# Performance work log

Hardware: AMD Instinct MI355X
Metric: run time of the kernel (lower is better)

The kernel has to match this reference:

```python
import jax, jax.numpy as jnp
import numpy as np

NUM_CODES = 8192
CODE_DIM = 256
BETA = 0.25


def setup_inputs() -> dict:
    key = jax.random.key(0)
    k1, k2 = jax.random.split(key)
    z_e = jax.random.normal(k1, (32, 1024, CODE_DIM), dtype=jnp.float32)
    # matches nn.init.uniform_(weight, -1/num_codes, 1/num_codes)
    codebook = jax.random.uniform(
        k2, (NUM_CODES, CODE_DIM), dtype=jnp.float32,
        minval=-1.0 / NUM_CODES, maxval=1.0 / NUM_CODES)
    return {"z_e": z_e, "codebook": codebook}


def reference(z_e, codebook):
    b, n, d = z_e.shape
    z_flat = z_e.reshape(-1, d)                       # [B*N, D]
    # squared L2 distance via ||z||^2 - 2 z.e + ||e||^2
    z_sq = jnp.sum(z_flat * z_flat, axis=1, keepdims=True)      # [B*N, 1]
    e_sq = jnp.sum(codebook * codebook, axis=1)[None, :]         # [1, K]
    ze = z_flat @ codebook.T                                     # [B*N, K]
    dist = z_sq - 2.0 * ze + e_sq
    codes_idx = jnp.argmin(dist, axis=1)                         # [B*N]
    z_q = codebook[codes_idx].reshape(b, n, d)
    # straight-through estimator
    z_q_st = z_e + jax.lax.stop_gradient(z_q - z_e)
    vq_loss = (jnp.mean((jax.lax.stop_gradient(z_q) - z_e) ** 2)
               + BETA * jnp.mean((z_q - jax.lax.stop_gradient(z_e)) ** 2))
    return z_q_st, vq_loss, codes_idx.reshape(b, n)
```

## Files before the change

### kernel.cpp

```cpp
#include <hip/hip_runtime.h>


#define NUM_CODES 8192
#define DIM 256
#define TOTAL_ROWS 32768
#define ROWS_PER_BLOCK 64
#define TILE_K 32
#define NCHUNK_HALF 128
#define OUT_LOSS_OFF 8388608
#define OUT_IDX_OFF 8388609
#define LOSS_SCALE (1.25 / 8388608.0)
#define DOT_MARGIN 3.5e-4f
#define CLIST_MAX 160

typedef __attribute__((ext_vector_type(8))) short bf16x8;
typedef __attribute__((ext_vector_type(4))) float f32x4;

#define AS1 __attribute__((address_space(1)))
#define AS3 __attribute__((address_space(3)))
static __device__ __forceinline__ void gload_lds16(const void* g, void* l) {
    __builtin_amdgcn_global_load_lds((const AS1 unsigned int*)(uintptr_t)g,
                                     (AS3 unsigned int*)(uintptr_t)l, 16, 0, 0);
}

static __device__ __forceinline__ unsigned short f2bf(float f) {
    union { float f; unsigned u; } v; v.f = f;
    return (unsigned short)((v.u + 0x7FFF + ((v.u >> 16) & 1)) >> 16);
}

static __device__ __forceinline__ float sq32(float v) {
    float s = v * v;
    asm("" : "+v"(s));
    return s;
}

static __device__ __forceinline__ float pairwise256_sq(
        const float* __restrict__ base, int l) {
    const int h = (l >> 3) & 1, j = l & 7;
    const float* p = base + h * 128 + j;
    float acc = sq32(p[0]);
    #pragma unroll
    for (int m = 1; m < 16; ++m) acc += sq32(p[m * 8]);
    acc += __shfl_xor(acc, 1);
    acc += __shfl_xor(acc, 2);
    acc += __shfl_xor(acc, 4);
    acc += __shfl_xor(acc, 8);
    return acc;
}

__global__ __launch_bounds__(64) void rowsq_kernel(const float* __restrict__ x,
                                                   float* __restrict__ sq) {
    const int l = threadIdx.x;
    const long row = ((long)blockIdx.x << 2) + (l >> 4);
    float s = pairwise256_sq(x + row * DIM, l);
    if ((l & 15) == 0) sq[row] = s;
}

__global__ __launch_bounds__(256) void cvt_swz_kernel(
        const float* __restrict__ cb, uint4* __restrict__ pbz) {
    const int o = blockIdx.x * 256 + threadIdx.x;
    const int ch = o >> 10, idx = o & 1023;
    const int c = idx >> 5, sw = idx & 31;
    const int s = sw ^ (c & 7);
    const float* p = cb + ((long)(ch * TILE_K + c) << 8) + s * 8;
    float4 a = *(const float4*)p, b = *(const float4*)(p + 4);
    union { unsigned short us[8]; uint4 v; } r;
    r.us[0] = f2bf(a.x); r.us[1] = f2bf(a.y); r.us[2] = f2bf(a.z); r.us[3] = f2bf(a.w);
    r.us[4] = f2bf(b.x); r.us[5] = f2bf(b.y); r.us[6] = f2bf(b.z); r.us[7] = f2bf(b.w);
    pbz[o] = r.v;
}

__global__ __launch_bounds__(128, 2) void vq_scan_kernel(
        const float* __restrict__ z, const float* __restrict__ cb,
        const uint4* __restrict__ pbz, const float* __restrict__ esq,
        unsigned long long* __restrict__ gwin) {
    __shared__ bf16x8 ct[2][TILE_K * 32];
    __shared__ float zsql[ROWS_PER_BLOCK];
    __shared__ unsigned clist[2][CLIST_MAX];
    __shared__ int ccnt[2];

    const int tid = threadIdx.x;
    const int w = tid >> 6, l = tid & 63;
    const int cl = l & 15, g = l >> 4;
    const int x7 = cl & 7;
    const int rowblk = blockIdx.x & 511;
    const int half = blockIdx.x >> 9;
    const int ch0 = half * NCHUNK_HALF;
    const long rowbase = (long)rowblk * ROWS_PER_BLOCK;
    const int wrowL = w * 32;

    if (l == 0) ccnt[w] = 0;

    #define STAGE(gch_, buf_) { \
        const char* gs_ = (const char*)pbz + ((long)(gch_) << 14) + (w << 10) + (l << 4); \
        char* ld_ = (char*)&ct[buf_][0] + (w << 10); \
        _Pragma("unroll") \
        for (int i_ = 0; i_ < 8; ++i_) \
            gload_lds16(gs_ + i_ * 2048, ld_ + i_ * 2048); \
    }

    STAGE(ch0, 0);

    bf16x8 af[2][8];
    #pragma unroll
    for (int t = 0; t < 2; ++t) {
        const long r = rowbase + wrowL + t * 16 + cl;
        #pragma unroll
        for (int ks = 0; ks < 8; ++ks) {
            const float* p = z + r * DIM + ks * 32 + g * 8;
            float4 a = *(const float4*)p, b = *(const float4*)(p + 4);
            bf16x8 v;
            v[0] = f2bf(a.x); v[1] = f2bf(a.y); v[2] = f2bf(a.z); v[3] = f2bf(a.w);
            v[4] = f2bf(b.x); v[5] = f2bf(b.y); v[6] = f2bf(b.z); v[7] = f2bf(b.w);
            af[t][ks] = v;
        }
    }
    #pragma unroll
    for (int p4 = 0; p4 < 8; ++p4) {
        const int r0 = wrowL + p4 * 4 + (l >> 4);
        float s = pairwise256_sq(z + (rowbase + r0) * DIM, l);
        if ((l & 15) == 0) zsql[r0] = s;
    }
    __syncthreads();

    unsigned k1a[8], k2a[8], k3a[8];
    #pragma unroll
    for (int i = 0; i < 8; ++i) { k1a[i] = 0u; k2a[i] = 0u; k3a[i] = 0u; }

    #define INSERT(rs_, sv_, kc_) { \
        unsigned u_ = __float_as_uint(sv_); \
        u_ ^= ((unsigned)((int)u_ >> 31)) | 0x80000000u; \
        u_ = (u_ & 0xFFFFE000u) | (kc_); \
        unsigned mx_ = k1a[rs_] > u_ ? k1a[rs_] : u_; \
        unsigned mn_ = k1a[rs_] > u_ ? u_ : k1a[rs_]; \
        k1a[rs_] = mx_; \
        unsigned mx2_ = k2a[rs_] > mn_ ? k2a[rs_] : mn_; \
        unsigned mn2_ = k2a[rs_] > mn_ ? mn_ : k2a[rs_]; \
        k2a[rs_] = mx2_; \
        k3a[rs_] = k3a[rs_] > mn2_ ? k3a[rs_] : mn2_; \
    }

    for (int ch = 0; ch < NCHUNK_HALF; ++ch) {
        const int buf = ch & 1;
        if (ch + 1 < NCHUNK_HALF) STAGE(ch0 + ch + 1, buf ^ 1);

        bf16x8 breg[16];
        #pragma unroll
        for (int ks = 0; ks < 8; ++ks)
            #pragma unroll
            for (int nt = 0; nt < 2; ++nt)
                breg[ks * 2 + nt] =
                    ct[buf][nt * 512 + cl * 32 + (((ks << 2) + g) ^ x7)];

        f32x4 acc[2][2];
        #pragma unroll
        for (int t = 0; t < 2; ++t)
            #pragma unroll
            for (int n = 0; n < 2; ++n) acc[t][n] = (f32x4){0.f, 0.f, 0.f, 0.f};
        #pragma unroll
        for (int ks = 0; ks < 8; ++ks) {
            #pragma unroll
            for (int nt = 0; nt < 2; ++nt) {
                acc[0][nt] = __builtin_amdgcn_mfma_f32_16x16x32_bf16(
                    af[0][ks], breg[ks * 2 + nt], acc[0][nt], 0, 0, 0);
                acc[1][nt] = __builtin_amdgcn_mfma_f32_16x16x32_bf16(
                    af[1][ks], breg[ks * 2 + nt], acc[1][nt], 0, 0, 0);
            }
        }

        const unsigned kc0 = (unsigned)((ch0 + ch) * TILE_K + cl);
        #pragma unroll
        for (int t = 0; t < 2; ++t)
            #pragma unroll
            for (int nt = 0; nt < 2; ++nt)
                #pragma unroll
                for (int r = 0; r < 4; ++r)
                    INSERT(t * 4 + r, acc[t][nt][r], nt ? (kc0 + 16) : kc0);

        __syncthreads();
    }

    #define COLLECT(rs_, T_, R_) { \
        unsigned gm_ = k1a[rs_]; \
        unsigned t_; \
        t_ = __shfl_xor(gm_, 1); gm_ = gm_ > t_ ? gm_ : t_; \
        t_ = __shfl_xor(gm_, 2); gm_ = gm_ > t_ ? gm_ : t_; \
        t_ = __shfl_xor(gm_, 4); gm_ = gm_ > t_ ? gm_ : t_; \
        t_ = __shfl_xor(gm_, 8); gm_ = gm_ > t_ ? gm_ : t_; \
        unsigned sb_ = (gm_ & 0x80000000u) ? (gm_ ^ 0x80000000u) : ~gm_; \
        float gs_ = __uint_as_float(sb_) - DOT_MARGIN; \
        unsigned tu_ = __float_as_uint(gs_); \
        tu_ ^= ((unsigned)((int)tu_ >> 31)) | 0x80000000u; \
        tu_ &= 0xFFFFE000u; \
        const unsigned rowp_ = (unsigned)(wrowL + T_ * 16 + g * 4 + R_) << 16; \
        if (k1a[rs_] >= tu_) { int p_ = atomicAdd(&ccnt[w], 1); \
            if (p_ < CLIST_MAX) clist[w][p_] = rowp_ | (k1a[rs_] & 0x1FFFu); } \
        if (k2a[rs_] >= tu_) { int p_ = atomicAdd(&ccnt[w], 1); \
            if (p_ < CLIST_MAX) clist[w][p_] = rowp_ | (k2a[rs_] & 0x1FFFu); } \
        if (k3a[rs_] >= tu_) { int p_ = atomicAdd(&ccnt[w], 1); \
            if (p_ < CLIST_MAX) clist[w][p_] = rowp_ | (k3a[rs_] & 0x1FFFu); } \
    }
    COLLECT(0, 0, 0); COLLECT(1, 0, 1); COLLECT(2, 0, 2); COLLECT(3, 0, 3);
    COLLECT(4, 1, 0); COLLECT(5, 1, 1); COLLECT(6, 1, 2); COLLECT(7, 1, 3);

    const int n = ccnt[w] < CLIST_MAX ? ccnt[w] : CLIST_MAX;
    for (int j = 0; j < n; ++j) {
        const unsigned e = clist[w][j];
        const int rowL = e >> 16;
        const int code = e & 0x1FFF;
        const long grow = rowbase + rowL;
        float4 zz = *(const float4*)(z + grow * DIM + l * 4);
        float4 cc = *(const float4*)(cb + (long)code * DIM + l * 4);
        double dd = (double)zz.x * cc.x + (double)zz.y * cc.y
                  + (double)zz.z * cc.z + (double)zz.w * cc.w;
        dd += __shfl_xor(dd, 1);
        dd += __shfl_xor(dd, 2);
        dd += __shfl_xor(dd, 4);
        dd += __shfl_xor(dd, 8);
        dd += __shfl_xor(dd, 16);
        dd += __shfl_xor(dd, 32);
        const float s = (zsql[rowL] - 2.0f * (float)dd) + esq[code];
        if (l == 0) {
            const unsigned long long p =
                ((unsigned long long)__float_as_uint(s) << 32) | (unsigned)code;
            atomicMin(&gwin[grow], p);
        }
    }
}

__global__ __launch_bounds__(256) void vq_out_kernel(
        const float* __restrict__ z, const float* __restrict__ cb,
        const unsigned long long* __restrict__ gwin,
        float* __restrict__ out, double* __restrict__ loss_acc) {
    const int tid = threadIdx.x;
    const int w = tid >> 6, l = tid & 63;
    const long rowbase = (long)blockIdx.x * ROWS_PER_BLOCK;
    double lacc = 0.0;
    #pragma unroll 1
    for (int i = 0; i < 16; ++i) {
        const long grow = rowbase + w * 16 + i;
        const int kw = (int)(gwin[grow] & 0x1FFFull);
        float4 zz = *(const float4*)(z + grow * DIM + l * 4);
        float4 cq = *(const float4*)(cb + (long)kw * DIM + l * 4);
        float4 oo;
        oo.x = zz.x + (cq.x - zz.x); oo.y = zz.y + (cq.y - zz.y);
        oo.z = zz.z + (cq.z - zz.z); oo.w = zz.w + (cq.w - zz.w);
        *(float4*)(out + grow * DIM + l * 4) = oo;
        if (l == 0) out[OUT_IDX_OFF + grow] = (float)kw;
        const double d0 = (double)cq.x - zz.x, d1 = (double)cq.y - zz.y;
        const double d2 = (double)cq.z - zz.z, d3 = (double)cq.w - zz.w;
        lacc += d0 * d0 + d1 * d1 + d2 * d2 + d3 * d3;
    }
    lacc += __shfl_xor(lacc, 1);
    lacc += __shfl_xor(lacc, 2);
    lacc += __shfl_xor(lacc, 4);
    lacc += __shfl_xor(lacc, 8);
    lacc += __shfl_xor(lacc, 16);
    lacc += __shfl_xor(lacc, 32);
    if (l == 0) atomicAdd(loss_acc, lacc);
}

__global__ void vq_finalize_kernel(const double* __restrict__ loss_acc,
                                   float* __restrict__ out) {
    out[OUT_LOSS_OFF] = (float)(*loss_acc * LOSS_SCALE);
}

extern "C" void kernel_launch(void* const* d_in, const int* in_sizes, int n_in,
                              void* d_out, int out_size, void* d_ws, size_t ws_size,
                              hipStream_t stream) {
    const float* z  = (const float*)d_in[0];
    const float* cb = (const float*)d_in[1];
    float* out = (float*)d_out;
    double* loss_acc = (double*)d_ws;
    float* esq = (float*)((char*)d_ws + 1024);
    unsigned long long* gwin =
        (unsigned long long*)((char*)d_ws + 65536);
    uint4* pbz = (uint4*)((char*)d_ws + 393216);

    hipMemsetAsync(d_ws, 0, 8, stream);
    hipMemsetAsync(gwin, 0xFF, TOTAL_ROWS * 8, stream);
    rowsq_kernel<<<NUM_CODES / 4, 64, 0, stream>>>(cb, esq);
    cvt_swz_kernel<<<NUM_CODES * TILE_K / 256, 256, 0, stream>>>(cb, pbz);
    vq_scan_kernel<<<1024, 128, 0, stream>>>(z, cb, pbz, esq, gwin);
    vq_out_kernel<<<TOTAL_ROWS / ROWS_PER_BLOCK, 256, 0, stream>>>(
        z, cb, gwin, out, loss_acc);
    vq_finalize_kernel<<<1, 1, 0, stream>>>(loss_acc, out);
}
```

Measured before the change: 354.2 us.

## Enlarge scan tile to 128 rows and split codebook into quarters

The scan kernel now gives each block 128 rows (64 per wave, four 16-row A tiles) and a quarter of the codebook, where before it had 64 rows and half the codebook. Each B fragment loaded from LDS is therefore reused across four MFMAs instead of two, which cuts LDS reads per MFMA. Accumulators start at a positive bias so the float bits can be compared as unsigned keys without the sign-flip transform, which shortens the top-3 insert path. The trade-offs are higher register pressure (af doubled, three key arrays of 16), a wider candidate margin and a larger candidate list, and correctness now depends on the bias keeping every dot product positive.

```diff
diff --git a/kernel.cpp b/kernel.cpp
--- a/kernel.cpp
+++ b/kernel.cpp
@@ -4,14 +4,16 @@
 #define NUM_CODES 8192
 #define DIM 256
 #define TOTAL_ROWS 32768
-#define ROWS_PER_BLOCK 64
+#define SCAN_ROWS 128
+#define OUT_ROWS 64
 #define TILE_K 32
-#define NCHUNK_HALF 128
+#define NCHUNK_Q 64
 #define OUT_LOSS_OFF 8388608
 #define OUT_IDX_OFF 8388609
 #define LOSS_SCALE (1.25 / 8388608.0)
-#define DOT_MARGIN 3.5e-4f
-#define CLIST_MAX 160
+#define DOT_MARGIN 5e-4f
+#define BIAS 0.0625f
+#define CLIST_MAX 448
 
 typedef __attribute__((ext_vector_type(8))) short bf16x8;
 typedef __attribute__((ext_vector_type(4))) float f32x4;
@@ -75,7 +77,7 @@
         const uint4* __restrict__ pbz, const float* __restrict__ esq,
         unsigned long long* __restrict__ gwin) {
     __shared__ bf16x8 ct[2][TILE_K * 32];
-    __shared__ float zsql[ROWS_PER_BLOCK];
+    __shared__ float zsql[SCAN_ROWS];
     __shared__ unsigned clist[2][CLIST_MAX];
     __shared__ int ccnt[2];
 
@@ -83,11 +85,11 @@
     const int w = tid >> 6, l = tid & 63;
     const int cl = l & 15, g = l >> 4;
     const int x7 = cl & 7;
-    const int rowblk = blockIdx.x & 511;
-    const int half = blockIdx.x >> 9;
-    const int ch0 = half * NCHUNK_HALF;
-    const long rowbase = (long)rowblk * ROWS_PER_BLOCK;
-    const int wrowL = w * 32;
+    const int rowblk = blockIdx.x & 255;
+    const int quarter = blockIdx.x >> 8;
+    const int ch0 = quarter * NCHUNK_Q;
+    const long rowbase = (long)rowblk * SCAN_ROWS;
+    const int wrowL = w * 64;
 
     if (l == 0) ccnt[w] = 0;
 
@@ -101,9 +103,16 @@
 
     STAGE(ch0, 0);
 
-    bf16x8 af[2][8];
-    #pragma unroll
-    for (int t = 0; t < 2; ++t) {
+    #pragma unroll
+    for (int p4 = 0; p4 < 16; ++p4) {
+        const int r0 = wrowL + p4 * 4 + (l >> 4);
+        float s = pairwise256_sq(z + (rowbase + r0) * DIM, l);
+        if ((l & 15) == 0) zsql[r0] = s;
+    }
+
+    bf16x8 af[4][8];
+    #pragma unroll
+    for (int t = 0; t < 4; ++t) {
         const long r = rowbase + wrowL + t * 16 + cl;
         #pragma unroll
         for (int ks = 0; ks < 8; ++ks) {
@@ -115,22 +124,14 @@
             af[t][ks] = v;
         }
     }
-    #pragma unroll
-    for (int p4 = 0; p4 < 8; ++p4) {
-        const int r0 = wrowL + p4 * 4 + (l >> 4);
-        float s = pairwise256_sq(z + (rowbase + r0) * DIM, l);
-        if ((l & 15) == 0) zsql[r0] = s;
-    }
     __syncthreads();
 
-    unsigned k1a[8], k2a[8], k3a[8];
-    #pragma unroll
-    for (int i = 0; i < 8; ++i) { k1a[i] = 0u; k2a[i] = 0u; k3a[i] = 0u; }
+    unsigned k1a[16], k2a[16], k3a[16];
+    #pragma unroll
+    for (int i = 0; i < 16; ++i) { k1a[i] = 0u; k2a[i] = 0u; k3a[i] = 0u; }
 
     #define INSERT(rs_, sv_, kc_) { \
-        unsigned u_ = __float_as_uint(sv_); \
-        u_ ^= ((unsigned)((int)u_ >> 31)) | 0x80000000u; \
-        u_ = (u_ & 0xFFFFE000u) | (kc_); \
+        unsigned u_ = (__float_as_uint(sv_) & 0xFFFFE000u) | (kc_); \
         unsigned mx_ = k1a[rs_] > u_ ? k1a[rs_] : u_; \
         unsigned mn_ = k1a[rs_] > u_ ? u_ : k1a[rs_]; \
         k1a[rs_] = mx_; \
@@ -140,43 +141,42 @@
         k3a[rs_] = k3a[rs_] > mn2_ ? k3a[rs_] : mn2_; \
     }
 
-    for (int ch = 0; ch < NCHUNK_HALF; ++ch) {
+    for (int ch = 0; ch < NCHUNK_Q; ++ch) {
         const int buf = ch & 1;
-        if (ch + 1 < NCHUNK_HALF) STAGE(ch0 + ch + 1, buf ^ 1);
-
-        bf16x8 breg[16];
+        if (ch + 1 < NCHUNK_Q) STAGE(ch0 + ch + 1, buf ^ 1);
+
+        const unsigned kc0 = (unsigned)((ch0 + ch) * TILE_K + cl);
         #pragma unroll
-        for (int ks = 0; ks < 8; ++ks)
-            #pragma unroll
-            for (int nt = 0; nt < 2; ++nt)
-                breg[ks * 2 + nt] =
-                    ct[buf][nt * 512 + cl * 32 + (((ks << 2) + g) ^ x7)];
-
-        f32x4 acc[2][2];
-        #pragma unroll
-        for (int t = 0; t < 2; ++t)
-            #pragma unroll
-            for (int n = 0; n < 2; ++n) acc[t][n] = (f32x4){0.f, 0.f, 0.f, 0.f};
-        #pragma unroll
-        for (int ks = 0; ks < 8; ++ks) {
-            #pragma unroll
-            for (int nt = 0; nt < 2; ++nt) {
-                acc[0][nt] = __builtin_amdgcn_mfma_f32_16x16x32_bf16(
-                    af[0][ks], breg[ks * 2 + nt], acc[0][nt], 0, 0, 0);
-                acc[1][nt] = __builtin_amdgcn_mfma_f32_16x16x32_bf16(
-                    af[1][ks], breg[ks * 2 + nt], acc[1][nt], 0, 0, 0);
+        for (int nt = 0; nt < 2; ++nt) {
+            bf16x8 breg[8];
+            #pragma unroll
+            for (int ks = 0; ks < 8; ++ks)
+                breg[ks] = ct[buf][nt * 512 + cl * 32 + (((ks << 2) + g) ^ x7)];
+
+            f32x4 acc[4];
+            #pragma unroll
+            for (int t = 0; t < 4; ++t)
+                acc[t] = (f32x4){BIAS, BIAS, BIAS, BIAS};
+            #pragma unroll
+            for (int ks = 0; ks < 8; ++ks) {
+                acc[0] = __builtin_amdgcn_mfma_f32_16x16x32_bf16(
+                    af[0][ks], breg[ks], acc[0], 0, 0, 0);
+                acc[1] = __builtin_amdgcn_mfma_f32_16x16x32_bf16(
+                    af[1][ks], breg[ks], acc[1], 0, 0, 0);
+                acc[2] = __builtin_amdgcn_mfma_f32_16x16x32_bf16(
+                    af[2][ks], breg[ks], acc[2], 0, 0, 0);
+                acc[3] = __builtin_amdgcn_mfma_f32_16x16x32_bf16(
+                    af[3][ks], breg[ks], acc[3], 0, 0, 0);
+            }
+            const unsigned kcn = nt ? (kc0 + 16) : kc0;
+            #pragma unroll
+            for (int t = 0; t < 4; ++t) {
+                INSERT(t * 4 + 0, acc[t][0], kcn);
+                INSERT(t * 4 + 1, acc[t][1], kcn);
+                INSERT(t * 4 + 2, acc[t][2], kcn);
+                INSERT(t * 4 + 3, acc[t][3], kcn);
             }
         }
-
-        const unsigned kc0 = (unsigned)((ch0 + ch) * TILE_K + cl);
-        #pragma unroll
-        for (int t = 0; t < 2; ++t)
-            #pragma unroll
-            for (int nt = 0; nt < 2; ++nt)
-                #pragma unroll
-                for (int r = 0; r < 4; ++r)
-                    INSERT(t * 4 + r, acc[t][nt][r], nt ? (kc0 + 16) : kc0);
-
         __syncthreads();
     }
 
@@ -187,21 +187,20 @@
         t_ = __shfl_xor(gm_, 2); gm_ = gm_ > t_ ? gm_ : t_; \
         t_ = __shfl_xor(gm_, 4); gm_ = gm_ > t_ ? gm_ : t_; \
         t_ = __shfl_xor(gm_, 8); gm_ = gm_ > t_ ? gm_ : t_; \
-        unsigned sb_ = (gm_ & 0x80000000u) ? (gm_ ^ 0x80000000u) : ~gm_; \
-        float gs_ = __uint_as_float(sb_) - DOT_MARGIN; \
-        unsigned tu_ = __float_as_uint(gs_); \
-        tu_ ^= ((unsigned)((int)tu_ >> 31)) | 0x80000000u; \
-        tu_ &= 0xFFFFE000u; \
+        float gs_ = __uint_as_float(gm_ & 0xFFFFE000u) - DOT_MARGIN; \
+        const unsigned thr_ = __float_as_uint(gs_) & 0xFFFFE000u; \
         const unsigned rowp_ = (unsigned)(wrowL + T_ * 16 + g * 4 + R_) << 16; \
-        if (k1a[rs_] >= tu_) { int p_ = atomicAdd(&ccnt[w], 1); \
+        if (k1a[rs_] >= thr_) { int p_ = atomicAdd(&ccnt[w], 1); \
             if (p_ < CLIST_MAX) clist[w][p_] = rowp_ | (k1a[rs_] & 0x1FFFu); } \
-        if (k2a[rs_] >= tu_) { int p_ = atomicAdd(&ccnt[w], 1); \
+        if (k2a[rs_] >= thr_) { int p_ = atomicAdd(&ccnt[w], 1); \
             if (p_ < CLIST_MAX) clist[w][p_] = rowp_ | (k2a[rs_] & 0x1FFFu); } \
-        if (k3a[rs_] >= tu_) { int p_ = atomicAdd(&ccnt[w], 1); \
+        if (k3a[rs_] >= thr_) { int p_ = atomicAdd(&ccnt[w], 1); \
             if (p_ < CLIST_MAX) clist[w][p_] = rowp_ | (k3a[rs_] & 0x1FFFu); } \
     }
-    COLLECT(0, 0, 0); COLLECT(1, 0, 1); COLLECT(2, 0, 2); COLLECT(3, 0, 3);
-    COLLECT(4, 1, 0); COLLECT(5, 1, 1); COLLECT(6, 1, 2); COLLECT(7, 1, 3);
+    COLLECT(0, 0, 0);  COLLECT(1, 0, 1);  COLLECT(2, 0, 2);  COLLECT(3, 0, 3);
+    COLLECT(4, 1, 0);  COLLECT(5, 1, 1);  COLLECT(6, 1, 2);  COLLECT(7, 1, 3);
+    COLLECT(8, 2, 0);  COLLECT(9, 2, 1);  COLLECT(10, 2, 2); COLLECT(11, 2, 3);
+    COLLECT(12, 3, 0); COLLECT(13, 3, 1); COLLECT(14, 3, 2); COLLECT(15, 3, 3);
 
     const int n = ccnt[w] < CLIST_MAX ? ccnt[w] : CLIST_MAX;
     for (int j = 0; j < n; ++j) {
@@ -234,7 +233,7 @@
         float* __restrict__ out, double* __restrict__ loss_acc) {
     const int tid = threadIdx.x;
     const int w = tid >> 6, l = tid & 63;
-    const long rowbase = (long)blockIdx.x * ROWS_PER_BLOCK;
+    const long rowbase = (long)blockIdx.x * OUT_ROWS;
     double lacc = 0.0;
     #pragma unroll 1
     for (int i = 0; i < 16; ++i) {
@@ -282,7 +281,7 @@
     rowsq_kernel<<<NUM_CODES / 4, 64, 0, stream>>>(cb, esq);
     cvt_swz_kernel<<<NUM_CODES * TILE_K / 256, 256, 0, stream>>>(cb, pbz);
     vq_scan_kernel<<<1024, 128, 0, stream>>>(z, cb, pbz, esq, gwin);
-    vq_out_kernel<<<TOTAL_ROWS / ROWS_PER_BLOCK, 256, 0, stream>>>(
+    vq_out_kernel<<<TOTAL_ROWS / OUT_ROWS, 256, 0, stream>>>(
         z, cb, gwin, out, loss_acc);
     vq_finalize_kernel<<<1, 1, 0, stream>>>(loss_acc, out);
 }
```

Result: slower. 622.1 us (+75.6%).
